# Kernel tuning notes

Hardware: AMD Instinct MI355X
Metric: run time of the kernel (lower is better)

The kernel has to match this reference:

```python
import jax, jax.numpy as jnp
import numpy as np

EPS_NORM = 1e-12  # F.normalize eps
EPS_LOG = 1e-8    # forward's default eps


def setup_inputs() -> dict:
    key = jax.random.key(0)
    x = jax.random.normal(key, (16384, 256), dtype=jnp.float32)
    return {"student_output": x}


def reference(student_output) -> jnp.ndarray:
    x = student_output
    # L2-normalize rows (F.normalize with p=2, eps=1e-12)
    norm = jnp.maximum(jnp.linalg.norm(x, axis=-1, keepdims=True), EPS_NORM)
    xn = x / norm
    # pairwise squared euclidean via gram: ||xi-xj||^2 = 2 - 2<xi,xj> for unit vectors
    gram = xn @ xn.T  # [B, B]
    sq = jnp.clip(2.0 - 2.0 * gram, 0.0)
    b = sq.shape[0]
    eye = jnp.eye(b, dtype=bool)
    # mask diagonal before sqrt (avoids 0-grad/nan issues) then set to +inf
    dist = jnp.sqrt(jnp.where(eye, 1.0, sq))
    dist = jnp.where(eye, jnp.inf, dist)
    min_dist = jnp.min(dist, axis=1)  # [B] distance to nearest neighbor
    loss = -jnp.mean(jnp.log(min_dist + EPS_LOG))
    return loss
```

## Files before the change

### kernel.cpp

```cpp
#include <hip/hip_runtime.h>
#include <hip/hip_bf16.h>
#include <math.h>


typedef __attribute__((ext_vector_type(8))) short bf16x8;
typedef __attribute__((ext_vector_type(16))) float f32x16;

#define NROWS 16384
#define NDIM  256
#define NBLK  256

__global__ __launch_bounds__(256) void knorm(const float* __restrict__ x,
                                             float* __restrict__ rn) {
    int wid = threadIdx.x >> 6, lane = threadIdx.x & 63;
    int row = blockIdx.x * 4 + wid;
    const float4* xr = (const float4*)(x + (size_t)row * NDIM);
    float4 v = xr[lane];
    float ss = v.x * v.x + v.y * v.y + v.z * v.z + v.w * v.w;
    #pragma unroll
    for (int m = 1; m < 64; m <<= 1) ss += __shfl_xor(ss, m, 64);
    if (lane == 0) rn[row] = 1.0f / fmaxf(sqrtf(ss), 1e-12f);
}

__device__ inline unsigned bf_rne(float f) {
    union { float f; unsigned u; } c; c.f = f;
    return (c.u + 0x7FFFu + ((c.u >> 16) & 1u)) >> 16;
}
__device__ inline unsigned pack2(float lo, float hi) {
    return bf_rne(lo) | (bf_rne(hi) << 16);
}

__global__ __launch_bounds__(256) void kpack(const float* __restrict__ x,
                                             const float* __restrict__ rn,
                                             uint4* __restrict__ F) {
    int g = blockIdx.x * 256 + threadIdx.x;
    int t32  = g >> 10;
    int rem  = g & 1023;
    int ks   = rem >> 6;
    int lane = rem & 63;
    int row  = t32 * 32 + (lane & 31);
    int kb   = ks * 16 + (lane >> 5) * 8;
    float s = rn[row];
    const float4* xr = (const float4*)(x + (size_t)row * NDIM + kb);
    float4 a = xr[0], b = xr[1];
    uint4 o;
    o.x = pack2(a.x * s, a.y * s);
    o.y = pack2(a.z * s, a.w * s);
    o.z = pack2(b.x * s, b.y * s);
    o.w = pack2(b.z * s, b.w * s);
    F[g] = o;
}

__device__ inline void stage16(const uint4* __restrict__ g, const uint4* l) {
    __builtin_amdgcn_global_load_lds(
        (const __attribute__((address_space(1))) unsigned*)g,
        (__attribute__((address_space(3))) unsigned*)l, 16, 0, 0);
}

__device__ inline unsigned fkey(float f) {
    unsigned u = __builtin_bit_cast(unsigned, f);
    return (u & 0x80000000u) ? ~u : (u | 0x80000000u);
}

template<int CTRL>
__device__ inline float dpp_rot(float x) {
    int xi = __builtin_bit_cast(int, x);
    int yi = __builtin_amdgcn_update_dpp(xi, xi, CTRL, 0xF, 0xF, false);
    return __builtin_bit_cast(float, yi);
}

__global__ __launch_bounds__(256, 1) void kmax(const bf16x8* __restrict__ F,
                                               unsigned* __restrict__ rowcand) {
    __shared__ uint4 sbuf[2][2048];
    __shared__ uint4 dump[64];

    const int tid  = threadIdx.x;
    const int wid  = tid >> 6;
    const int lane = tid & 63;
    const int L    = lane & 31;
    const int hi   = lane >> 5;
    const uint4* F4 = (const uint4*)F;

    const int b    = ((blockIdx.x & 7) << 5) | (blockIdx.x >> 3);
    const int u0   = (b * 65) >> 1;
    const int uend = ((b + 1) * 65) >> 1;

    int cib = 0;
    while (2 * (cib + 1) * (129 - (cib + 1)) <= u0) ++cib;
    int cjp = 4 * cib + (u0 - 2 * cib * (129 - cib));

    bf16x8 bfr0[16], bfr1[16];
    int lib = cib;
    {
        int it = cib * 8 + 2 * wid;
        #pragma unroll
        for (int ks = 0; ks < 16; ++ks) {
            bfr0[ks] = F[(it + 0) * 1024 + ks * 64 + lane];
            bfr1[ks] = F[(it + 1) * 1024 + ks * 64 + lane];
        }
    }

    int sib = cib, sjp = cjp;
    {
        const uint4* gp = F4 + (size_t)cjp * 2048;
        #pragma unroll
        for (int q = 0; q < 8; ++q)
            stage16(gp + q * 256 + tid, &sbuf[0][q * 256 + wid * 64]);
    }
    atomicMax(&rowcand[0], 0u);

    float rm0[16], rm1[16];
    #pragma unroll
    for (int r = 0; r < 16; ++r) { rm0[r] = -1e30f; rm1[r] = -1e30f; }

    const bool dvalid = (((L >> 2) & 1) == hi);
    const int  dreg   = (L & 3) | ((L >> 3) << 2);
    const f32x16 zc = {0.f};

    auto flush_i = [&](int fib) {
        #pragma unroll
        for (int r = 0; r < 16; ++r) {
            float a = rm0[r];
            a = fmaxf(a, dpp_rot<0x121>(a));
            a = fmaxf(a, dpp_rot<0x122>(a));
            a = fmaxf(a, dpp_rot<0x124>(a));
            a = fmaxf(a, dpp_rot<0x128>(a));
            rm0[r] = fmaxf(a, __shfl_xor(a, 16, 64));
            float c = rm1[r];
            c = fmaxf(c, dpp_rot<0x121>(c));
            c = fmaxf(c, dpp_rot<0x122>(c));
            c = fmaxf(c, dpp_rot<0x124>(c));
            c = fmaxf(c, dpp_rot<0x128>(c));
            rm1[r] = fmaxf(c, __shfl_xor(c, 16, 64));
        }
        float v0 = rm0[0], v1 = rm1[0];
        #pragma unroll
        for (int r = 1; r < 16; ++r) {
            v0 = (dreg == r) ? rm0[r] : v0;
            v1 = (dreg == r) ? rm1[r] : v1;
        }
        if (dvalid) {
            int base = fib * 256 + wid * 64;
            atomicMax(&rowcand[base + L],      fkey(v0));
            atomicMax(&rowcand[base + 32 + L], fkey(v1));
        }
    };

    int bsel = 0;
    auto stepc = [](int& ib, int& jp) {
        if (++jp == 256) { if (ib < 63) { ++ib; jp = 4 * ib; } else jp = 255; }
    };

    for (int s = u0; s < uend; ++s) {
        asm volatile("s_waitcnt vmcnt(1)" ::: "memory");
        __builtin_amdgcn_s_barrier();
        __builtin_amdgcn_sched_barrier(0);

        if (cib != lib) {
            int it = cib * 8 + 2 * wid;
            #pragma unroll
            for (int ks = 0; ks < 16; ++ks) {
                bfr0[ks] = F[(it + 0) * 1024 + ks * 64 + lane];
                bfr1[ks] = F[(it + 1) * 1024 + ks * 64 + lane];
            }
            lib = cib;
        }
        const int  mjp = cjp;
        const int  mib = cib;
        const bool mpd = (cjp == cib * 4 + wid);

        const uint4* sb = &sbuf[bsel][0];
        f32x16 c00, c01, c10, c11;
        {
            bf16x8 af0 = *(const bf16x8*)(sb + lane);
            bf16x8 af1 = *(const bf16x8*)(sb + 1024 + lane);
            c00 = __builtin_amdgcn_mfma_f32_32x32x16_bf16(bfr0[0], af0, zc, 0, 0, 0);
            c10 = __builtin_amdgcn_mfma_f32_32x32x16_bf16(bfr1[0], af0, zc, 0, 0, 0);
            c01 = __builtin_amdgcn_mfma_f32_32x32x16_bf16(bfr0[0], af1, zc, 0, 0, 0);
            c11 = __builtin_amdgcn_mfma_f32_32x32x16_bf16(bfr1[0], af1, zc, 0, 0, 0);
        }
        #pragma unroll
        for (int ks = 1; ks < 16; ++ks) {
            bf16x8 af0 = *(const bf16x8*)(sb + ks * 64 + lane);
            bf16x8 af1 = *(const bf16x8*)(sb + 1024 + ks * 64 + lane);
            c00 = __builtin_amdgcn_mfma_f32_32x32x16_bf16(bfr0[ks], af0, c00, 0, 0, 0);
            c10 = __builtin_amdgcn_mfma_f32_32x32x16_bf16(bfr1[ks], af0, c10, 0, 0, 0);
            c01 = __builtin_amdgcn_mfma_f32_32x32x16_bf16(bfr0[ks], af1, c01, 0, 0, 0);
            c11 = __builtin_amdgcn_mfma_f32_32x32x16_bf16(bfr1[ks], af1, c11, 0, 0, 0);
        }

        stepc(sib, sjp);
        {
            const uint4* gp = F4 + (size_t)sjp * 2048;
            uint4* dst = &sbuf[bsel ^ 1][0];
            #pragma unroll
            for (int q = 0; q < 8; ++q)
                stage16(gp + q * 256 + tid, dst + q * 256 + wid * 64);
        }

        float jm0 = -1e30f, jm1 = -1e30f;
        if (mpd) {
            #pragma unroll
            for (int r = 0; r < 16; ++r) {
                float v00 = c00[r], v11 = c11[r];
                if (dvalid && r == dreg) { v00 = -1e30f; v11 = -1e30f; }
                rm0[r] = fmaxf(rm0[r], fmaxf(v00, c01[r]));
                rm1[r] = fmaxf(rm1[r], fmaxf(c10[r], v11));
                jm0 = fmaxf(jm0, fmaxf(v00, c10[r]));
                jm1 = fmaxf(jm1, fmaxf(c01[r], v11));
            }
        } else {
            #pragma unroll
            for (int r = 0; r < 16; ++r) {
                rm0[r] = fmaxf(rm0[r], fmaxf(c00[r], c01[r]));
                rm1[r] = fmaxf(rm1[r], fmaxf(c10[r], c11[r]));
                jm0 = fmaxf(jm0, fmaxf(c00[r], c10[r]));
                jm1 = fmaxf(jm1, fmaxf(c01[r], c11[r]));
            }
        }
        jm0 = fmaxf(jm0, __shfl_xor(jm0, 32, 64));
        jm1 = fmaxf(jm1, __shfl_xor(jm1, 32, 64));
        float js = hi ? jm1 : jm0;
        atomicMax(&rowcand[mjp * 64 + lane], fkey(js));

        stepc(cib, cjp);
        if (cib != mib) {
            flush_i(mib);
            #pragma unroll
            for (int r = 0; r < 16; ++r) { rm0[r] = -1e30f; rm1[r] = -1e30f; }
        }
        bsel ^= 1;
    }
    flush_i(lib);
}

__global__ __launch_bounds__(256) void kloss1(const unsigned* __restrict__ rowcand,
                                              float* __restrict__ partial) {
    int i = blockIdx.x * 256 + threadIdx.x;
    unsigned k = rowcand[i];
    unsigned u = (k & 0x80000000u) ? (k ^ 0x80000000u) : ~k;
    float gv = __builtin_bit_cast(float, u);
    float d = sqrtf(fmaxf(2.f - 2.f * gv, 0.f));
    float acc = logf(d + 1e-8f);
    #pragma unroll
    for (int m = 1; m < 64; m <<= 1) acc += __shfl_xor(acc, m, 64);
    __shared__ float p[4];
    int wid = threadIdx.x >> 6, lane = threadIdx.x & 63;
    if (lane == 0) p[wid] = acc;
    __syncthreads();
    if (threadIdx.x == 0)
        partial[blockIdx.x] = (p[0] + p[1]) + (p[2] + p[3]);
}

__global__ __launch_bounds__(64) void kloss2(const float* __restrict__ partial,
                                             float* __restrict__ out) {
    float acc = partial[threadIdx.x];
    #pragma unroll
    for (int m = 1; m < 64; m <<= 1) acc += __shfl_xor(acc, m, 64);
    if (threadIdx.x == 0) out[0] = -acc / (float)NROWS;
}

extern "C" void kernel_launch(void* const* d_in, const int* in_sizes, int n_in,
                              void* d_out, int out_size, void* d_ws, size_t ws_size,
                              hipStream_t stream) {
    const float* x = (const float*)d_in[0];
    float* out = (float*)d_out;
    char* ws = (char*)d_ws;

    uint4*    F       = (uint4*)ws;
    float*    rn      = (float*)(ws + 8u * 1024u * 1024u);
    unsigned* rowcand = (unsigned*)(ws + 8u * 1024u * 1024u + 65536u);
    float*    partial = (float*)(ws + 8u * 1024u * 1024u + 131072u);

    hipMemsetAsync(rowcand, 0, NROWS * sizeof(unsigned), stream);
    knorm<<<NROWS / 4, 256, 0, stream>>>(x, rn);
    kpack<<<(NROWS * NDIM / 8) / 256, 256, 0, stream>>>(x, rn, F);
    kmax <<<NBLK, 256, 0, stream>>>((const bf16x8*)F, rowcand);
    kloss1<<<64, 256, 0, stream>>>(rowcand, partial);
    kloss2<<<1, 64, 0, stream>>>(partial, out);
}
```

Measured before the change: 100.4 us.

## Fuse norm/pack/memset and widen gram tile to 256x128 per step

Merges the memset, row-norm and bf16 pack kernels into one kernel that zeros rowcand and computes norms in shared memory per 32-row tile. The main kmax kernel now processes 128 columns per step instead of 64, with 8 MFMA accumulators per wave and a 64KB double-buffered LDS stage, halving the number of steps and barriers. Staging of the next tile is issued before the MFMAs of the current tile. This cuts launch overhead and per-step sync cost, but raises register pressure and LDS use, and the diagonal-masking logic becomes more complex.

```diff
diff --git a/kernel.cpp b/kernel.cpp
--- a/kernel.cpp
+++ b/kernel.cpp
@@ -10,18 +10,6 @@
 #define NDIM  256
 #define NBLK  256
 
-__global__ __launch_bounds__(256) void knorm(const float* __restrict__ x,
-                                             float* __restrict__ rn) {
-    int wid = threadIdx.x >> 6, lane = threadIdx.x & 63;
-    int row = blockIdx.x * 4 + wid;
-    const float4* xr = (const float4*)(x + (size_t)row * NDIM);
-    float4 v = xr[lane];
-    float ss = v.x * v.x + v.y * v.y + v.z * v.z + v.w * v.w;
-    #pragma unroll
-    for (int m = 1; m < 64; m <<= 1) ss += __shfl_xor(ss, m, 64);
-    if (lane == 0) rn[row] = 1.0f / fmaxf(sqrtf(ss), 1e-12f);
-}
-
 __device__ inline unsigned bf_rne(float f) {
     union { float f; unsigned u; } c; c.f = f;
     return (c.u + 0x7FFFu + ((c.u >> 16) & 1u)) >> 16;
@@ -30,25 +18,47 @@
     return bf_rne(lo) | (bf_rne(hi) << 16);
 }
 
-__global__ __launch_bounds__(256) void kpack(const float* __restrict__ x,
-                                             const float* __restrict__ rn,
-                                             uint4* __restrict__ F) {
-    int g = blockIdx.x * 256 + threadIdx.x;
-    int t32  = g >> 10;
-    int rem  = g & 1023;
-    int ks   = rem >> 6;
-    int lane = rem & 63;
-    int row  = t32 * 32 + (lane & 31);
-    int kb   = ks * 16 + (lane >> 5) * 8;
-    float s = rn[row];
-    const float4* xr = (const float4*)(x + (size_t)row * NDIM + kb);
-    float4 a = xr[0], b = xr[1];
-    uint4 o;
-    o.x = pack2(a.x * s, a.y * s);
-    o.y = pack2(a.z * s, a.w * s);
-    o.z = pack2(b.x * s, b.y * s);
-    o.w = pack2(b.z * s, b.w * s);
-    F[g] = o;
+__global__ __launch_bounds__(256) void knp(const float* __restrict__ x,
+                                           uint4* __restrict__ F,
+                                           unsigned* __restrict__ rowcand) {
+    __shared__ float rnorm[32];
+    const int t32 = blockIdx.x;
+    const int tid = threadIdx.x;
+
+    if (tid < 32) rowcand[t32 * 32 + tid] = 0u;
+
+    int row = tid >> 3;
+    int c0  = (tid & 7) * 32;
+    const float4* xr = (const float4*)(x + ((size_t)t32 * 32 + row) * NDIM + c0);
+    float ss = 0.f;
+    #pragma unroll
+    for (int q = 0; q < 8; ++q) {
+        float4 v = xr[q];
+        ss += v.x * v.x + v.y * v.y + v.z * v.z + v.w * v.w;
+    }
+    ss += __shfl_xor(ss, 1, 64);
+    ss += __shfl_xor(ss, 2, 64);
+    ss += __shfl_xor(ss, 4, 64);
+    if ((tid & 7) == 0) rnorm[row] = 1.0f / fmaxf(sqrtf(ss), 1e-12f);
+    __syncthreads();
+
+    #pragma unroll
+    for (int q = 0; q < 4; ++q) {
+        int c    = q * 256 + tid;
+        int ks   = c >> 6;
+        int lane = c & 63;
+        int r    = lane & 31;
+        int kb   = ks * 16 + (lane >> 5) * 8;
+        float s  = rnorm[r];
+        const float4* xp = (const float4*)(x + ((size_t)t32 * 32 + r) * NDIM + kb);
+        float4 a = xp[0], b2 = xp[1];
+        uint4 o;
+        o.x = pack2(a.x * s, a.y * s);
+        o.y = pack2(a.z * s, a.w * s);
+        o.z = pack2(b2.x * s, b2.y * s);
+        o.w = pack2(b2.z * s, b2.w * s);
+        F[(size_t)t32 * 1024 + c] = o;
+    }
 }
 
 __device__ inline void stage16(const uint4* __restrict__ g, const uint4* l) {
@@ -71,8 +81,7 @@
 
 __global__ __launch_bounds__(256, 1) void kmax(const bf16x8* __restrict__ F,
                                                unsigned* __restrict__ rowcand) {
-    __shared__ uint4 sbuf[2][2048];
-    __shared__ uint4 dump[64];
+    __shared__ uint4 sbuf[2][4096];
 
     const int tid  = threadIdx.x;
     const int wid  = tid >> 6;
@@ -82,12 +91,12 @@
     const uint4* F4 = (const uint4*)F;
 
     const int b    = ((blockIdx.x & 7) << 5) | (blockIdx.x >> 3);
-    const int u0   = (b * 65) >> 1;
-    const int uend = ((b + 1) * 65) >> 1;
+    const int u0   = (b * 65) >> 2;
+    const int uend = ((b + 1) * 65) >> 2;
 
     int cib = 0;
-    while (2 * (cib + 1) * (129 - (cib + 1)) <= u0) ++cib;
-    int cjp = 4 * cib + (u0 - 2 * cib * (129 - cib));
+    while ((cib + 1) * (128 - cib) <= u0) ++cib;
+    int cjq = 2 * cib + (u0 - cib * (129 - cib));
 
     bf16x8 bfr0[16], bfr1[16];
     int lib = cib;
@@ -100,11 +109,10 @@
         }
     }
 
-    int sib = cib, sjp = cjp;
     {
-        const uint4* gp = F4 + (size_t)cjp * 2048;
-        #pragma unroll
-        for (int q = 0; q < 8; ++q)
+        const uint4* gp = F4 + (size_t)cjq * 4096;
+        #pragma unroll
+        for (int q = 0; q < 16; ++q)
             stage16(gp + q * 256 + tid, &sbuf[0][q * 256 + wid * 64]);
     }
     atomicMax(&rowcand[0], 0u);
@@ -147,10 +155,6 @@
     };
 
     int bsel = 0;
-    auto stepc = [](int& ib, int& jp) {
-        if (++jp == 256) { if (ib < 63) { ++ib; jp = 4 * ib; } else jp = 255; }
-    };
-
     for (int s = u0; s < uend; ++s) {
         asm volatile("s_waitcnt vmcnt(1)" ::: "memory");
         __builtin_amdgcn_s_barrier();
@@ -165,71 +169,99 @@
             }
             lib = cib;
         }
-        const int  mjp = cjp;
-        const int  mib = cib;
-        const bool mpd = (cjp == cib * 4 + wid);
+
+        int nib = cib, njq = cjq + 1;
+        if (njq == 128) { if (nib < 63) { ++nib; njq = 2 * nib; } else njq = 127; }
+        {
+            const uint4* gp = F4 + (size_t)njq * 4096;
+            uint4* dst = &sbuf[bsel ^ 1][0];
+            #pragma unroll
+            for (int q = 0; q < 16; ++q)
+                stage16(gp + q * 256 + tid, dst + q * 256 + wid * 64);
+        }
 
         const uint4* sb = &sbuf[bsel][0];
-        f32x16 c00, c01, c10, c11;
+        f32x16 c00, c01, c02, c03, c10, c11, c12, c13;
         {
-            bf16x8 af0 = *(const bf16x8*)(sb + lane);
-            bf16x8 af1 = *(const bf16x8*)(sb + 1024 + lane);
-            c00 = __builtin_amdgcn_mfma_f32_32x32x16_bf16(bfr0[0], af0, zc, 0, 0, 0);
-            c10 = __builtin_amdgcn_mfma_f32_32x32x16_bf16(bfr1[0], af0, zc, 0, 0, 0);
-            c01 = __builtin_amdgcn_mfma_f32_32x32x16_bf16(bfr0[0], af1, zc, 0, 0, 0);
-            c11 = __builtin_amdgcn_mfma_f32_32x32x16_bf16(bfr1[0], af1, zc, 0, 0, 0);
+            bf16x8 a0 = *(const bf16x8*)(sb + lane);
+            bf16x8 a1 = *(const bf16x8*)(sb + 1024 + lane);
+            bf16x8 a2 = *(const bf16x8*)(sb + 2048 + lane);
+            bf16x8 a3 = *(const bf16x8*)(sb + 3072 + lane);
+            c00 = __builtin_amdgcn_mfma_f32_32x32x16_bf16(bfr0[0], a0, zc, 0, 0, 0);
+            c10 = __builtin_amdgcn_mfma_f32_32x32x16_bf16(bfr1[0], a0, zc, 0, 0, 0);
+            c01 = __builtin_amdgcn_mfma_f32_32x32x16_bf16(bfr0[0], a1, zc, 0, 0, 0);
+            c11 = __builtin_amdgcn_mfma_f32_32x32x16_bf16(bfr1[0], a1, zc, 0, 0, 0);
+            c02 = __builtin_amdgcn_mfma_f32_32x32x16_bf16(bfr0[0], a2, zc, 0, 0, 0);
+            c12 = __builtin_amdgcn_mfma_f32_32x32x16_bf16(bfr1[0], a2, zc, 0, 0, 0);
+            c03 = __builtin_amdgcn_mfma_f32_32x32x16_bf16(bfr0[0], a3, zc, 0, 0, 0);
+            c13 = __builtin_amdgcn_mfma_f32_32x32x16_bf16(bfr1[0], a3, zc, 0, 0, 0);
         }
         #pragma unroll
         for (int ks = 1; ks < 16; ++ks) {
-            bf16x8 af0 = *(const bf16x8*)(sb + ks * 64 + lane);
-            bf16x8 af1 = *(const bf16x8*)(sb + 1024 + ks * 64 + lane);
-            c00 = __builtin_amdgcn_mfma_f32_32x32x16_bf16(bfr0[ks], af0, c00, 0, 0, 0);
-            c10 = __builtin_amdgcn_mfma_f32_32x32x16_bf16(bfr1[ks], af0, c10, 0, 0, 0);
-            c01 = __builtin_amdgcn_mfma_f32_32x32x16_bf16(bfr0[ks], af1, c01, 0, 0, 0);
-            c11 = __builtin_amdgcn_mfma_f32_32x32x16_bf16(bfr1[ks], af1, c11, 0, 0, 0);
-        }
-
-        stepc(sib, sjp);
-        {
-            const uint4* gp = F4 + (size_t)sjp * 2048;
-            uint4* dst = &sbuf[bsel ^ 1][0];
-            #pragma unroll
-            for (int q = 0; q < 8; ++q)
-                stage16(gp + q * 256 + tid, dst + q * 256 + wid * 64);
-        }
-
-        float jm0 = -1e30f, jm1 = -1e30f;
-        if (mpd) {
-            #pragma unroll
-            for (int r = 0; r < 16; ++r) {
-                float v00 = c00[r], v11 = c11[r];
-                if (dvalid && r == dreg) { v00 = -1e30f; v11 = -1e30f; }
-                rm0[r] = fmaxf(rm0[r], fmaxf(v00, c01[r]));
-                rm1[r] = fmaxf(rm1[r], fmaxf(c10[r], v11));
-                jm0 = fmaxf(jm0, fmaxf(v00, c10[r]));
-                jm1 = fmaxf(jm1, fmaxf(c01[r], v11));
-            }
+            bf16x8 a0 = *(const bf16x8*)(sb + ks * 64 + lane);
+            bf16x8 a1 = *(const bf16x8*)(sb + 1024 + ks * 64 + lane);
+            bf16x8 a2 = *(const bf16x8*)(sb + 2048 + ks * 64 + lane);
+            bf16x8 a3 = *(const bf16x8*)(sb + 3072 + ks * 64 + lane);
+            c00 = __builtin_amdgcn_mfma_f32_32x32x16_bf16(bfr0[ks], a0, c00, 0, 0, 0);
+            c10 = __builtin_amdgcn_mfma_f32_32x32x16_bf16(bfr1[ks], a0, c10, 0, 0, 0);
+            c01 = __builtin_amdgcn_mfma_f32_32x32x16_bf16(bfr0[ks], a1, c01, 0, 0, 0);
+            c11 = __builtin_amdgcn_mfma_f32_32x32x16_bf16(bfr1[ks], a1, c11, 0, 0, 0);
+            c02 = __builtin_amdgcn_mfma_f32_32x32x16_bf16(bfr0[ks], a2, c02, 0, 0, 0);
+            c12 = __builtin_amdgcn_mfma_f32_32x32x16_bf16(bfr1[ks], a2, c12, 0, 0, 0);
+            c03 = __builtin_amdgcn_mfma_f32_32x32x16_bf16(bfr0[ks], a3, c03, 0, 0, 0);
+            c13 = __builtin_amdgcn_mfma_f32_32x32x16_bf16(bfr1[ks], a3, c13, 0, 0, 0);
+        }
+
+        const int  dq      = cjq - 2 * cib;
+        const bool hasdiag = (dq <= 1) && (dq == (wid >> 1));
+        const int  jd0     = 2 * wid - 4 * dq;
+        const int  jd1     = jd0 + 1;
+        float jm0 = -1e30f, jm1 = -1e30f, jm2 = -1e30f, jm3 = -1e30f;
+
+#define EPI_R(r, MASKED)                                                      \
+        {                                                                     \
+            float a0 = c00[r], a1 = c01[r], a2 = c02[r], a3 = c03[r];         \
+            float b0 = c10[r], b1 = c11[r], b2 = c12[r], b3 = c13[r];         \
+            if (MASKED) {                                                     \
+                bool dr = dvalid && ((r) == dreg);                            \
+                if (dr && jd0 == 0) a0 = -1e30f;                              \
+                if (dr && jd0 == 1) a1 = -1e30f;                              \
+                if (dr && jd0 == 2) a2 = -1e30f;                              \
+                if (dr && jd0 == 3) a3 = -1e30f;                              \
+                if (dr && jd1 == 1) b1 = -1e30f;                              \
+                if (dr && jd1 == 2) b2 = -1e30f;                              \
+                if (dr && jd1 == 3) b3 = -1e30f;                              \
+            }                                                                 \
+            rm0[r] = fmaxf(rm0[r], fmaxf(fmaxf(a0, a1), fmaxf(a2, a3)));      \
+            rm1[r] = fmaxf(rm1[r], fmaxf(fmaxf(b0, b1), fmaxf(b2, b3)));      \
+            jm0 = fmaxf(jm0, fmaxf(a0, b0));                                  \
+            jm1 = fmaxf(jm1, fmaxf(a1, b1));                                  \
+            jm2 = fmaxf(jm2, fmaxf(a2, b2));                                  \
+            jm3 = fmaxf(jm3, fmaxf(a3, b3));                                  \
+        }
+        if (hasdiag) {
+            #pragma unroll
+            for (int r = 0; r < 16; ++r) EPI_R(r, true)
         } else {
             #pragma unroll
-            for (int r = 0; r < 16; ++r) {
-                rm0[r] = fmaxf(rm0[r], fmaxf(c00[r], c01[r]));
-                rm1[r] = fmaxf(rm1[r], fmaxf(c10[r], c11[r]));
-                jm0 = fmaxf(jm0, fmaxf(c00[r], c10[r]));
-                jm1 = fmaxf(jm1, fmaxf(c01[r], c11[r]));
-            }
-        }
+            for (int r = 0; r < 16; ++r) EPI_R(r, false)
+        }
+#undef EPI_R
         jm0 = fmaxf(jm0, __shfl_xor(jm0, 32, 64));
         jm1 = fmaxf(jm1, __shfl_xor(jm1, 32, 64));
-        float js = hi ? jm1 : jm0;
-        atomicMax(&rowcand[mjp * 64 + lane], fkey(js));
-
-        stepc(cib, cjp);
-        if (cib != mib) {
-            flush_i(mib);
+        jm2 = fmaxf(jm2, __shfl_xor(jm2, 32, 64));
+        jm3 = fmaxf(jm3, __shfl_xor(jm3, 32, 64));
+        float jsA = hi ? jm1 : jm0;
+        float jsB = hi ? jm3 : jm2;
+        atomicMax(&rowcand[cjq * 128 + lane],      fkey(jsA));
+        atomicMax(&rowcand[cjq * 128 + 64 + lane], fkey(jsB));
+
+        if (nib != cib) {
+            flush_i(cib);
             #pragma unroll
             for (int r = 0; r < 16; ++r) { rm0[r] = -1e30f; rm1[r] = -1e30f; }
         }
-        bsel ^= 1;
+        cib = nib; cjq = njq; bsel ^= 1;
     }
     flush_i(lib);
 }
@@ -268,14 +300,11 @@
     char* ws = (char*)d_ws;
 
     uint4*    F       = (uint4*)ws;
-    float*    rn      = (float*)(ws + 8u * 1024u * 1024u);
     unsigned* rowcand = (unsigned*)(ws + 8u * 1024u * 1024u + 65536u);
     float*    partial = (float*)(ws + 8u * 1024u * 1024u + 131072u);
 
-    hipMemsetAsync(rowcand, 0, NROWS * sizeof(unsigned), stream);
-    knorm<<<NROWS / 4, 256, 0, stream>>>(x, rn);
-    kpack<<<(NROWS * NDIM / 8) / 256, 256, 0, stream>>>(x, rn, F);
-    kmax <<<NBLK, 256, 0, stream>>>((const bf16x8*)F, rowcand);
+    knp   <<<NROWS / 32, 256, 0, stream>>>(x, F, rowcand);
+    kmax  <<<NBLK, 256, 0, stream>>>((const bf16x8*)F, rowcand);
     kloss1<<<64, 256, 0, stream>>>(rowcand, partial);
     kloss2<<<1, 64, 0, stream>>>(partial, out);
 }
```

Result: faster. 97.71 us (-2.6%).
